# Kernel optimization log

Hardware: AMD Instinct MI355X
Metric: run time of the kernel (lower is better)

## Reference

```python
import jax, jax.numpy as jnp
import numpy as np

NUM_ITER = 5
ALPHA = 5.0   # spatial bandwidth, bilateral kernel
BETA = 5.0    # feature bandwidth, bilateral kernel
GAMMA = 5.0   # spatial bandwidth, spatial kernel
W_1 = 1.0
W_2 = 1.0


def setup_inputs() -> dict:
    key = jax.random.key(0)
    k1, k2 = jax.random.split(key)
    B, C, X, Y, Z = 1, 4, 32, 16, 16
    log_unary = jax.random.normal(k1, (B, C, X, Y, Z), dtype=jnp.float32)
    features_pairwise = jax.random.normal(k2, (B, 2, X, Y, Z), dtype=jnp.float32)
    # Potts-model compatibility: ones minus identity, [C_out, C_in] (conv1d kernel size 1)
    compatibility_weights = (jnp.ones((C, C)) - jnp.eye(C)).astype(jnp.float32)
    return {"log_unary": log_unary, "features_pairwise": features_pairwise,
            "compatibility_weights": compatibility_weights}


def _gauss_kernel(f):
    # f: [B, D, N] feature vectors; dense Gaussian filter matrix K_ij = exp(-||f_i-f_j||^2/2)
    sq = jnp.sum(f * f, axis=1)  # [B, N]
    d2 = sq[:, :, None] + sq[:, None, :] - 2.0 * jnp.einsum('bdn,bdm->bnm', f, f)
    return jnp.exp(-0.5 * jnp.maximum(d2, 0.0))  # [B, N, N]


def reference(log_unary, features_pairwise, compatibility_weights):
    B, C, X, Y, Z = log_unary.shape
    N = X * Y * Z
    lu = log_unary.reshape(B, C, N)
    q = jax.nn.softmax(lu, axis=1)

    gx, gy, gz = jnp.meshgrid(jnp.arange(X), jnp.arange(Y), jnp.arange(Z), indexing='ij')
    spatial = jnp.stack([gx, gy, gz], axis=0).astype(jnp.float32).reshape(1, 3, N)
    spatial = jnp.broadcast_to(spatial, (B, 3, N))
    img_fea = features_pairwise.reshape(B, features_pairwise.shape[1], N)

    f1 = jnp.concatenate([spatial / ALPHA, img_fea / BETA], axis=1)  # bilateral features
    f2 = spatial / GAMMA                                             # spatial features

    K1 = _gauss_kernel(f1)
    K2 = _gauss_kernel(f2)
    # norm = filter(ones) = row sums; scale = rsqrt(norm)
    scale1 = jax.lax.rsqrt(jnp.sum(K1, axis=2))[:, None, :]  # [B,1,N]
    scale2 = jax.lax.rsqrt(jnp.sum(K2, axis=2))[:, None, :]

    for _ in range(NUM_ITER):
        q1 = jnp.einsum('bnm,bcm->bcn', K1, q * scale1) * scale1
        q2 = jnp.einsum('bnm,bcm->bcn', K2, q * scale2) * scale2
        q_comb = W_1 * q1 + W_2 * q2
        q_update = jnp.einsum('oc,bcn->bon', compatibility_weights, q_comb)
        q = jax.nn.softmax(lu - q_update, axis=1)

    return q.reshape(B, C, X, Y, Z)
```

## Files before the change

kernel.cpp:

```cpp
#include <hip/hip_runtime.h>
#include <math.h>


constexpr int   NT    = 8192;
constexpr float SQL2E = 1.2011224087864498f;
constexpr float LOG2E = 1.4426950408889634f;
constexpr float INVA  = 0.2f * SQL2E;

constexpr int R_M = 0, R_U1 = 32, R_U2 = 36, R_S1 = 40, R_S2 = 41, R_CV = 42;

static __device__ __forceinline__ float ex2(float x) {
    return __builtin_amdgcn_exp2f(x);
}

__constant__ float INVSQF[7] = {1.f, 1.f, 0.70710678f, 0.40824829f,
                                0.20412415f, 0.09128709f, 0.03726780f};

__global__ __launch_bounds__(256) void k_setup(const float* __restrict__ feat,
                                               float* __restrict__ W) {
    int n = blockIdx.x * 256 + threadIdx.x;
    float g0 = feat[n] * 0.2f, g1 = feat[NT + n] * 0.2f;
    float eg = ex2(-0.5f * LOG2E * (g0*g0 + g1*g1));
    float p0[7], p1[7];
    p0[0] = 1.f; p1[0] = 1.f;
#pragma unroll
    for (int i = 1; i < 7; i++) { p0[i] = p0[i-1]*g0; p1[i] = p1[i-1]*g1; }
    int ab = 0;
#pragma unroll
    for (int k = 0; k <= 6; k++)
#pragma unroll
        for (int a = k; a >= 0; a--) {
            int b = k - a;
            W[(R_M + ab)*NT + n] = eg * p0[a]*INVSQF[a] * p1[b]*INVSQF[b];
            ab++;
        }
    int x = n >> 8, y = (n >> 4) & 15, z = n & 15;
    float Sx = 0.f, Sy = 0.f, Sz = 0.f;
    for (int j = 0; j < 32; j++) { float d = (float)(x-j)*INVA; Sx += ex2(-0.5f*d*d); }
    for (int j = 0; j < 16; j++) { float d = (float)(y-j)*INVA; Sy += ex2(-0.5f*d*d); }
    for (int j = 0; j < 16; j++) { float d = (float)(z-j)*INVA; Sz += ex2(-0.5f*d*d); }
    W[R_S2*NT + n] = rsqrtf(Sx * Sy * Sz);
}

__global__ __launch_bounds__(256) void k_conv(const float* __restrict__ W,
                                              float* __restrict__ Wout, int mode) {
    __shared__ float SP[512 * 17];
    const int idx = blockIdx.x;
    const int tid = threadIdx.x;
    if (mode == 0) {
        const float* src = W + (R_M + idx) * NT;
        for (int s = tid; s < NT; s += 256)
            SP[(s >> 4)*17 + (s & 15)] = src[s];
    } else if (idx < 112) {
        const float* Mr = W + (R_M + (idx >> 2)) * NT;
        const float* ur = W + (R_U1 + (idx & 3)) * NT;
        for (int s = tid; s < NT; s += 256)
            SP[(s >> 4)*17 + (s & 15)] = Mr[s] * ur[s];
    } else {
        const float* ur = W + (R_U2 + (idx - 112)) * NT;
        for (int s = tid; s < NT; s += 256)
            SP[(s >> 4)*17 + (s & 15)] = ur[s];
    }
    float g32[32];
#pragma unroll
    for (int d = 0; d < 32; d++) { float t = d * INVA; g32[d] = ex2(-0.5f*t*t); }
    __syncthreads();
#pragma unroll
    for (int rr = 0; rr < 2; rr++) {
        int r = tid + rr * 256;
        float v[16], acc[16];
#pragma unroll
        for (int z = 0; z < 16; z++) { v[z] = SP[r*17 + z]; acc[z] = 0.f; }
#pragma unroll
        for (int zp = 0; zp < 16; zp++)
#pragma unroll
            for (int z = 0; z < 16; z++) {
                int d = (z > zp) ? (z - zp) : (zp - z);
                acc[z] = fmaf(g32[d], v[zp], acc[z]);
            }
#pragma unroll
        for (int z = 0; z < 16; z++) SP[r*17 + z] = acc[z];
    }
    __syncthreads();
#pragma unroll
    for (int rr = 0; rr < 2; rr++) {
        int r = tid + rr * 256;
        int x = r >> 4, z = r & 15;
        int base = x * 272 + z;
        float v[16], acc[16];
#pragma unroll
        for (int y = 0; y < 16; y++) { v[y] = SP[base + y*17]; acc[y] = 0.f; }
#pragma unroll
        for (int yp = 0; yp < 16; yp++)
#pragma unroll
            for (int y = 0; y < 16; y++) {
                int d = (y > yp) ? (y - yp) : (yp - y);
                acc[y] = fmaf(g32[d], v[yp], acc[y]);
            }
#pragma unroll
        for (int y = 0; y < 16; y++) SP[base + y*17] = acc[y];
    }
    __syncthreads();
    {
        int base = (tid >> 4) * 17 + (tid & 15);
        float v[32], acc[32];
#pragma unroll
        for (int xp = 0; xp < 32; xp++) { v[xp] = SP[base + xp*272]; acc[xp] = 0.f; }
#pragma unroll
        for (int xp = 0; xp < 32; xp++)
#pragma unroll
            for (int x = 0; x < 32; x++) {
                int d = (x > xp) ? (x - xp) : (xp - x);
                acc[x] = fmaf(g32[d], v[xp], acc[x]);
            }
        float* outp = Wout + (R_CV + idx) * NT;
#pragma unroll
        for (int x = 0; x < 32; x++) outp[x*256 + tid] = acc[x];
    }
}

__global__ __launch_bounds__(256) void k_init(float* __restrict__ W,
                                              const float* __restrict__ lu) {
    int n = blockIdx.x * 256 + threadIdx.x;
    float rs = 0.f;
#pragma unroll
    for (int ab = 0; ab < 28; ab++)
        rs = fmaf(W[(R_M+ab)*NT + n], W[(R_CV+ab)*NT + n], rs);
    float s1 = rsqrtf(rs);
    float s2 = W[R_S2*NT + n];
    W[R_S1*NT + n] = s1;
    float l0 = lu[n], l1 = lu[NT+n], l2 = lu[2*NT+n], l3 = lu[3*NT+n];
    float mx = fmaxf(fmaxf(l0,l1), fmaxf(l2,l3));
    float q0 = __expf(l0-mx), q1 = __expf(l1-mx), q2 = __expf(l2-mx), q3 = __expf(l3-mx);
    float inv = 1.f / (q0+q1+q2+q3);
    q0*=inv; q1*=inv; q2*=inv; q3*=inv;
    W[(R_U1+0)*NT+n]=q0*s1; W[(R_U1+1)*NT+n]=q1*s1; W[(R_U1+2)*NT+n]=q2*s1; W[(R_U1+3)*NT+n]=q3*s1;
    W[(R_U2+0)*NT+n]=q0*s2; W[(R_U2+1)*NT+n]=q1*s2; W[(R_U2+2)*NT+n]=q2*s2; W[(R_U2+3)*NT+n]=q3*s2;
}

__global__ __launch_bounds__(256) void k_fuse(float* __restrict__ W,
        const float* __restrict__ lu, const float* __restrict__ compat,
        float* __restrict__ out) {
    int n = blockIdx.x * 256 + threadIdx.x;
    float s1 = W[R_S1*NT + n], s2 = W[R_S2*NT + n];
    float q1[4] = {0.f, 0.f, 0.f, 0.f};
#pragma unroll
    for (int ab = 0; ab < 28; ab++) {
        float m = W[(R_M+ab)*NT + n];
#pragma unroll
        for (int c = 0; c < 4; c++)
            q1[c] = fmaf(m, W[(R_CV + ab*4 + c)*NT + n], q1[c]);
    }
    float comb[4];
#pragma unroll
    for (int c = 0; c < 4; c++)
        comb[c] = s1 * q1[c] + s2 * W[(R_CV + 112 + c)*NT + n];
    float q[4];
#pragma unroll
    for (int o = 0; o < 4; o++) {
        float upd = 0.f;
#pragma unroll
        for (int c = 0; c < 4; c++) upd = fmaf(compat[o*4+c], comb[c], upd);
        q[o] = lu[o*NT+n] - upd;
    }
    float mx = fmaxf(fmaxf(q[0],q[1]), fmaxf(q[2],q[3]));
    float sum = 0.f;
#pragma unroll
    for (int c = 0; c < 4; c++) { q[c] = __expf(q[c]-mx); sum += q[c]; }
    float inv = 1.f / sum;
#pragma unroll
    for (int c = 0; c < 4; c++) {
        q[c] *= inv;
        out[c*NT+n]        = q[c];
        W[(R_U1+c)*NT+n]   = q[c]*s1;
        W[(R_U2+c)*NT+n]   = q[c]*s2;
    }
}

extern "C" void kernel_launch(void* const* d_in, const int* in_sizes, int n_in,
                              void* d_out, int out_size, void* d_ws, size_t ws_size,
                              hipStream_t stream) {
    const float* lu     = (const float*)d_in[0];
    const float* feat   = (const float*)d_in[1];
    const float* compat = (const float*)d_in[2];
    float* out = (float*)d_out;
    float* W   = (float*)d_ws;

    k_setup<<<dim3(32), dim3(256), 0, stream>>>(feat, W);
    k_conv <<<dim3(28), dim3(256), 0, stream>>>(W, W, 0);
    k_init <<<dim3(32), dim3(256), 0, stream>>>(W, lu);
    for (int it = 0; it < 5; it++) {
        k_conv<<<dim3(116), dim3(256), 0, stream>>>(W, W, 1);
        k_fuse<<<dim3(32),  dim3(256), 0, stream>>>(W, lu, compat, out);
    }
}
```

Baseline: 146.3 us.

## Fuse whole CRF pipeline into one cooperative kernel with grid syncs

Replaces the 13 separate kernel launches with a single cooperative persistent kernel of 116 blocks that uses grid.sync between the setup, init, conv and fuse phases. The setup moment computation is folded into the conv blocks, and fuse work is spread over all blocks at about 71 points each. It also skips the intermediate output writes except on the last iteration. The goal is to remove per-launch overhead and gaps between kernels, at the cost of grid-wide barrier latency and fewer active threads in the per-point phases; the old multi-kernel path remains as a fallback if the cooperative launch fails.

```diff
diff --git a/kernel.cpp b/kernel.cpp
--- a/kernel.cpp
+++ b/kernel.cpp
@@ -1,13 +1,18 @@
 #include <hip/hip_runtime.h>
+#include <hip/hip_cooperative_groups.h>
 #include <math.h>
 
+namespace cg = cooperative_groups;
+
 
 constexpr int   NT    = 8192;
+constexpr float LOG2E = 1.4426950408889634f;
 constexpr float SQL2E = 1.2011224087864498f;
-constexpr float LOG2E = 1.4426950408889634f;
 constexpr float INVA  = 0.2f * SQL2E;
 
 constexpr int R_M = 0, R_U1 = 32, R_U2 = 36, R_S1 = 40, R_S2 = 41, R_CV = 42;
+constexpr int NBLK = 116;
+constexpr int PPB  = (NT + NBLK - 1) / NBLK;
 
 static __device__ __forceinline__ float ex2(float x) {
     return __builtin_amdgcn_exp2f(x);
@@ -15,6 +20,190 @@
 
 __constant__ float INVSQF[7] = {1.f, 1.f, 0.70710678f, 0.40824829f,
                                 0.20412415f, 0.09128709f, 0.03726780f};
+__constant__ int AB_A[28] = {0, 1,0, 2,1,0, 3,2,1,0, 4,3,2,1,0,
+                             5,4,3,2,1,0, 6,5,4,3,2,1,0};
+__constant__ int AB_B[28] = {0, 0,1, 0,1,2, 0,1,2,3, 0,1,2,3,4,
+                             0,1,2,3,4,5, 0,1,2,3,4,5,6};
+
+static __device__ __forceinline__ void conv3d_store(float* SP,
+                                                    float* __restrict__ outp,
+                                                    int tid) {
+    float g32[32];
+#pragma unroll
+    for (int d = 0; d < 32; d++) { float t = d * INVA; g32[d] = ex2(-0.5f*t*t); }
+    __syncthreads();
+#pragma unroll
+    for (int rr = 0; rr < 2; rr++) {
+        int r = tid + rr * 256;
+        float v[16], acc[16];
+#pragma unroll
+        for (int z = 0; z < 16; z++) { v[z] = SP[r*17 + z]; acc[z] = 0.f; }
+#pragma unroll
+        for (int zp = 0; zp < 16; zp++)
+#pragma unroll
+            for (int z = 0; z < 16; z++) {
+                int d = (z > zp) ? (z - zp) : (zp - z);
+                acc[z] = fmaf(g32[d], v[zp], acc[z]);
+            }
+#pragma unroll
+        for (int z = 0; z < 16; z++) SP[r*17 + z] = acc[z];
+    }
+    __syncthreads();
+#pragma unroll
+    for (int rr = 0; rr < 2; rr++) {
+        int r = tid + rr * 256;
+        int x = r >> 4, z = r & 15;
+        int base = x * 272 + z;
+        float v[16], acc[16];
+#pragma unroll
+        for (int y = 0; y < 16; y++) { v[y] = SP[base + y*17]; acc[y] = 0.f; }
+#pragma unroll
+        for (int yp = 0; yp < 16; yp++)
+#pragma unroll
+            for (int y = 0; y < 16; y++) {
+                int d = (y > yp) ? (y - yp) : (yp - y);
+                acc[y] = fmaf(g32[d], v[yp], acc[y]);
+            }
+#pragma unroll
+        for (int y = 0; y < 16; y++) SP[base + y*17] = acc[y];
+    }
+    __syncthreads();
+    {
+        int base = (tid >> 4) * 17 + (tid & 15);
+        float v[32], acc[32];
+#pragma unroll
+        for (int xp = 0; xp < 32; xp++) { v[xp] = SP[base + xp*272]; acc[xp] = 0.f; }
+#pragma unroll
+        for (int xp = 0; xp < 32; xp++)
+#pragma unroll
+            for (int x = 0; x < 32; x++) {
+                int d = (x > xp) ? (x - xp) : (xp - x);
+                acc[x] = fmaf(g32[d], v[xp], acc[x]);
+            }
+#pragma unroll
+        for (int x = 0; x < 32; x++) outp[x*256 + tid] = acc[x];
+    }
+}
+
+static __device__ __forceinline__ void init_point(float* __restrict__ W,
+                                                  const float* __restrict__ lu,
+                                                  int n) {
+    float rs = 0.f;
+#pragma unroll
+    for (int ab = 0; ab < 28; ab++)
+        rs = fmaf(W[(R_M+ab)*NT + n], W[(R_CV+ab)*NT + n], rs);
+    float s1 = rsqrtf(rs);
+    float s2 = W[R_S2*NT + n];
+    W[R_S1*NT + n] = s1;
+    float l0 = lu[n], l1 = lu[NT+n], l2 = lu[2*NT+n], l3 = lu[3*NT+n];
+    float mx = fmaxf(fmaxf(l0,l1), fmaxf(l2,l3));
+    float q0 = __expf(l0-mx), q1 = __expf(l1-mx), q2 = __expf(l2-mx), q3 = __expf(l3-mx);
+    float inv = 1.f / (q0+q1+q2+q3);
+    q0*=inv; q1*=inv; q2*=inv; q3*=inv;
+    W[(R_U1+0)*NT+n]=q0*s1; W[(R_U1+1)*NT+n]=q1*s1; W[(R_U1+2)*NT+n]=q2*s1; W[(R_U1+3)*NT+n]=q3*s1;
+    W[(R_U2+0)*NT+n]=q0*s2; W[(R_U2+1)*NT+n]=q1*s2; W[(R_U2+2)*NT+n]=q2*s2; W[(R_U2+3)*NT+n]=q3*s2;
+}
+
+static __device__ __forceinline__ void fuse_point(float* __restrict__ W,
+        const float* __restrict__ lu, const float* __restrict__ compat,
+        float* __restrict__ out, int n, int last) {
+    float s1 = W[R_S1*NT + n], s2 = W[R_S2*NT + n];
+    float q1[4] = {0.f, 0.f, 0.f, 0.f};
+#pragma unroll
+    for (int ab = 0; ab < 28; ab++) {
+        float m = W[(R_M+ab)*NT + n];
+#pragma unroll
+        for (int c = 0; c < 4; c++)
+            q1[c] = fmaf(m, W[(R_CV + ab*4 + c)*NT + n], q1[c]);
+    }
+    float comb[4];
+#pragma unroll
+    for (int c = 0; c < 4; c++)
+        comb[c] = s1 * q1[c] + s2 * W[(R_CV + 112 + c)*NT + n];
+    float q[4];
+#pragma unroll
+    for (int o = 0; o < 4; o++) {
+        float upd = 0.f;
+#pragma unroll
+        for (int c = 0; c < 4; c++) upd = fmaf(compat[o*4+c], comb[c], upd);
+        q[o] = lu[o*NT+n] - upd;
+    }
+    float mx = fmaxf(fmaxf(q[0],q[1]), fmaxf(q[2],q[3]));
+    float sum = 0.f;
+#pragma unroll
+    for (int c = 0; c < 4; c++) { q[c] = __expf(q[c]-mx); sum += q[c]; }
+    float inv = 1.f / sum;
+    if (last) {
+#pragma unroll
+        for (int c = 0; c < 4; c++) out[c*NT+n] = q[c] * inv;
+    } else {
+#pragma unroll
+        for (int c = 0; c < 4; c++) {
+            float qq = q[c] * inv;
+            W[(R_U1+c)*NT+n] = qq*s1;
+            W[(R_U2+c)*NT+n] = qq*s2;
+        }
+    }
+}
+
+__global__ __launch_bounds__(256) void k_crf_all(const float* __restrict__ lu,
+        const float* __restrict__ feat, const float* __restrict__ compat,
+        float* __restrict__ out, float* __restrict__ W) {
+    cg::grid_group grid = cg::this_grid();
+    __shared__ float SP[512 * 17];
+    const int bid = blockIdx.x, tid = threadIdx.x;
+
+    if (bid < 28) {
+        const int a = AB_A[bid], b = AB_B[bid];
+        const float ca = INVSQF[a], cb = INVSQF[b];
+        for (int s = tid; s < NT; s += 256) {
+            float g0 = feat[s] * 0.2f, g1 = feat[NT + s] * 0.2f;
+            float eg = ex2(-0.5f * LOG2E * (g0*g0 + g1*g1));
+            float pa = 1.f;
+            for (int i = 0; i < a; i++) pa *= g0;
+            float pb = 1.f;
+            for (int i = 0; i < b; i++) pb *= g1;
+            float v = eg * pa * ca * pb * cb;
+            W[(R_M + bid)*NT + s] = v;
+            SP[(s >> 4)*17 + (s & 15)] = v;
+        }
+        conv3d_store(SP, W + (R_CV + bid)*NT, tid);
+    } else {
+        const int nb = (bid - 28) * 94 + tid;
+        if (tid < 94 && nb < NT) {
+            int x = nb >> 8, y = (nb >> 4) & 15, z = nb & 15;
+            float Sx = 0.f, Sy = 0.f, Sz = 0.f;
+            for (int j = 0; j < 32; j++) { float d = (float)(x-j)*INVA; Sx += ex2(-0.5f*d*d); }
+            for (int j = 0; j < 16; j++) { float d = (float)(y-j)*INVA; Sy += ex2(-0.5f*d*d); }
+            for (int j = 0; j < 16; j++) { float d = (float)(z-j)*INVA; Sz += ex2(-0.5f*d*d); }
+            W[R_S2*NT + nb] = rsqrtf(Sx * Sy * Sz);
+        }
+    }
+    grid.sync();
+
+    { int n = bid * PPB + tid; if (tid < PPB && n < NT) init_point(W, lu, n); }
+    grid.sync();
+
+    for (int it = 0; it < 5; ++it) {
+        {
+            const int idx = bid;
+            if (idx < 112) {
+                const float* Mr = W + (R_M + (idx >> 2))*NT;
+                const float* ur = W + (R_U1 + (idx & 3))*NT;
+                for (int s = tid; s < NT; s += 256)
+                    SP[(s >> 4)*17 + (s & 15)] = Mr[s] * ur[s];
+            } else {
+                const float* ur = W + (R_U2 + (idx - 112))*NT;
+                for (int s = tid; s < NT; s += 256)
+                    SP[(s >> 4)*17 + (s & 15)] = ur[s];
+            }
+            conv3d_store(SP, W + (R_CV + idx)*NT, tid);
+        }
+        grid.sync();
+        { int n = bid * PPB + tid; if (tid < PPB && n < NT) fuse_point(W, lu, compat, out, n, it == 4); }
+        grid.sync();
+    }
+}
 
 __global__ __launch_bounds__(256) void k_setup(const float* __restrict__ feat,
                                                float* __restrict__ W) {
@@ -61,120 +250,20 @@
         for (int s = tid; s < NT; s += 256)
             SP[(s >> 4)*17 + (s & 15)] = ur[s];
     }
-    float g32[32];
-#pragma unroll
-    for (int d = 0; d < 32; d++) { float t = d * INVA; g32[d] = ex2(-0.5f*t*t); }
-    __syncthreads();
-#pragma unroll
-    for (int rr = 0; rr < 2; rr++) {
-        int r = tid + rr * 256;
-        float v[16], acc[16];
-#pragma unroll
-        for (int z = 0; z < 16; z++) { v[z] = SP[r*17 + z]; acc[z] = 0.f; }
-#pragma unroll
-        for (int zp = 0; zp < 16; zp++)
-#pragma unroll
-            for (int z = 0; z < 16; z++) {
-                int d = (z > zp) ? (z - zp) : (zp - z);
-                acc[z] = fmaf(g32[d], v[zp], acc[z]);
-            }
-#pragma unroll
-        for (int z = 0; z < 16; z++) SP[r*17 + z] = acc[z];
-    }
-    __syncthreads();
-#pragma unroll
-    for (int rr = 0; rr < 2; rr++) {
-        int r = tid + rr * 256;
-        int x = r >> 4, z = r & 15;
-        int base = x * 272 + z;
-        float v[16], acc[16];
-#pragma unroll
-        for (int y = 0; y < 16; y++) { v[y] = SP[base + y*17]; acc[y] = 0.f; }
-#pragma unroll
-        for (int yp = 0; yp < 16; yp++)
-#pragma unroll
-            for (int y = 0; y < 16; y++) {
-                int d = (y > yp) ? (y - yp) : (yp - y);
-                acc[y] = fmaf(g32[d], v[yp], acc[y]);
-            }
-#pragma unroll
-        for (int y = 0; y < 16; y++) SP[base + y*17] = acc[y];
-    }
-    __syncthreads();
-    {
-        int base = (tid >> 4) * 17 + (tid & 15);
-        float v[32], acc[32];
-#pragma unroll
-        for (int xp = 0; xp < 32; xp++) { v[xp] = SP[base + xp*272]; acc[xp] = 0.f; }
-#pragma unroll
-        for (int xp = 0; xp < 32; xp++)
-#pragma unroll
-            for (int x = 0; x < 32; x++) {
-                int d = (x > xp) ? (x - xp) : (xp - x);
-                acc[x] = fmaf(g32[d], v[xp], acc[x]);
-            }
-        float* outp = Wout + (R_CV + idx) * NT;
-#pragma unroll
-        for (int x = 0; x < 32; x++) outp[x*256 + tid] = acc[x];
-    }
+    conv3d_store(SP, Wout + (R_CV + idx)*NT, tid);
 }
 
 __global__ __launch_bounds__(256) void k_init(float* __restrict__ W,
                                               const float* __restrict__ lu) {
     int n = blockIdx.x * 256 + threadIdx.x;
-    float rs = 0.f;
-#pragma unroll
-    for (int ab = 0; ab < 28; ab++)
-        rs = fmaf(W[(R_M+ab)*NT + n], W[(R_CV+ab)*NT + n], rs);
-    float s1 = rsqrtf(rs);
-    float s2 = W[R_S2*NT + n];
-    W[R_S1*NT + n] = s1;
-    float l0 = lu[n], l1 = lu[NT+n], l2 = lu[2*NT+n], l3 = lu[3*NT+n];
-    float mx = fmaxf(fmaxf(l0,l1), fmaxf(l2,l3));
-    float q0 = __expf(l0-mx), q1 = __expf(l1-mx), q2 = __expf(l2-mx), q3 = __expf(l3-mx);
-    float inv = 1.f / (q0+q1+q2+q3);
-    q0*=inv; q1*=inv; q2*=inv; q3*=inv;
-    W[(R_U1+0)*NT+n]=q0*s1; W[(R_U1+1)*NT+n]=q1*s1; W[(R_U1+2)*NT+n]=q2*s1; W[(R_U1+3)*NT+n]=q3*s1;
-    W[(R_U2+0)*NT+n]=q0*s2; W[(R_U2+1)*NT+n]=q1*s2; W[(R_U2+2)*NT+n]=q2*s2; W[(R_U2+3)*NT+n]=q3*s2;
+    init_point(W, lu, n);
 }
 
 __global__ __launch_bounds__(256) void k_fuse(float* __restrict__ W,
         const float* __restrict__ lu, const float* __restrict__ compat,
-        float* __restrict__ out) {
+        float* __restrict__ out, int last) {
     int n = blockIdx.x * 256 + threadIdx.x;
-    float s1 = W[R_S1*NT + n], s2 = W[R_S2*NT + n];
-    float q1[4] = {0.f, 0.f, 0.f, 0.f};
-#pragma unroll
-    for (int ab = 0; ab < 28; ab++) {
-        float m = W[(R_M+ab)*NT + n];
-#pragma unroll
-        for (int c = 0; c < 4; c++)
-            q1[c] = fmaf(m, W[(R_CV + ab*4 + c)*NT + n], q1[c]);
-    }
-    float comb[4];
-#pragma unroll
-    for (int c = 0; c < 4; c++)
-        comb[c] = s1 * q1[c] + s2 * W[(R_CV + 112 + c)*NT + n];
-    float q[4];
-#pragma unroll
-    for (int o = 0; o < 4; o++) {
-        float upd = 0.f;
-#pragma unroll
-        for (int c = 0; c < 4; c++) upd = fmaf(compat[o*4+c], comb[c], upd);
-        q[o] = lu[o*NT+n] - upd;
-    }
-    float mx = fmaxf(fmaxf(q[0],q[1]), fmaxf(q[2],q[3]));
-    float sum = 0.f;
-#pragma unroll
-    for (int c = 0; c < 4; c++) { q[c] = __expf(q[c]-mx); sum += q[c]; }
-    float inv = 1.f / sum;
-#pragma unroll
-    for (int c = 0; c < 4; c++) {
-        q[c] *= inv;
-        out[c*NT+n]        = q[c];
-        W[(R_U1+c)*NT+n]   = q[c]*s1;
-        W[(R_U2+c)*NT+n]   = q[c]*s2;
-    }
+    fuse_point(W, lu, compat, out, n, last);
 }
 
 extern "C" void kernel_launch(void* const* d_in, const int* in_sizes, int n_in,
@@ -186,11 +275,17 @@
     float* out = (float*)d_out;
     float* W   = (float*)d_ws;
 
-    k_setup<<<dim3(32), dim3(256), 0, stream>>>(feat, W);
-    k_conv <<<dim3(28), dim3(256), 0, stream>>>(W, W, 0);
-    k_init <<<dim3(32), dim3(256), 0, stream>>>(W, lu);
-    for (int it = 0; it < 5; it++) {
-        k_conv<<<dim3(116), dim3(256), 0, stream>>>(W, W, 1);
-        k_fuse<<<dim3(32),  dim3(256), 0, stream>>>(W, lu, compat, out);
-    }
-}
+    void* args[] = {(void*)&lu, (void*)&feat, (void*)&compat, (void*)&out, (void*)&W};
+    hipError_t rc = hipLaunchCooperativeKernel((const void*)k_crf_all,
+                                               dim3(NBLK), dim3(256), args, 0, stream);
+    if (rc != hipSuccess) {
+        (void)hipGetLastError();
+        k_setup<<<dim3(32), dim3(256), 0, stream>>>(feat, W);
+        k_conv <<<dim3(28), dim3(256), 0, stream>>>(W, W, 0);
+        k_init <<<dim3(32), dim3(256), 0, stream>>>(W, lu);
+        for (int it = 0; it < 5; it++) {
+            k_conv<<<dim3(116), dim3(256), 0, stream>>>(W, W, 1);
+            k_fuse<<<dim3(32),  dim3(256), 0, stream>>>(W, lu, compat, out, it == 4);
+        }
+    }
+}
```

Measured after the change: 443.7 us. 203% more time.

## Fuse setup into separable conv, use 512-thread conv blocks with vectorized loads

Applied to the files above, without the earlier changes.

Merges the setup and initial convolution kernels into one phase that computes each moment map and convolves it directly from shared memory. The spatial normalization moves into the init kernel. The separable 3D Gaussian convolution now runs with 512 threads per block, one row per thread, and the x pass is split into two halves. This raises parallelism and cuts per-thread register work. Conv input loads use float4, and the final fuse skips the workspace writes, giving one fewer launch and less memory traffic at the cost of more barrier-synchronized threads per block.

```diff
diff --git a/kernel.cpp b/kernel.cpp
--- a/kernel.cpp
+++ b/kernel.cpp
@@ -3,8 +3,8 @@
 
 
 constexpr int   NT    = 8192;
+constexpr float LOG2E = 1.4426950408889634f;
 constexpr float SQL2E = 1.2011224087864498f;
-constexpr float LOG2E = 1.4426950408889634f;
 constexpr float INVA  = 0.2f * SQL2E;
 
 constexpr int R_M = 0, R_U1 = 32, R_U2 = 36, R_S1 = 40, R_S2 = 41, R_CV = 42;
@@ -15,119 +15,120 @@
 
 __constant__ float INVSQF[7] = {1.f, 1.f, 0.70710678f, 0.40824829f,
                                 0.20412415f, 0.09128709f, 0.03726780f};
-
-__global__ __launch_bounds__(256) void k_setup(const float* __restrict__ feat,
-                                               float* __restrict__ W) {
+__constant__ int AB_A[28] = {0, 1,0, 2,1,0, 3,2,1,0, 4,3,2,1,0,
+                             5,4,3,2,1,0, 6,5,4,3,2,1,0};
+__constant__ int AB_B[28] = {0, 0,1, 0,1,2, 0,1,2,3, 0,1,2,3,4,
+                             0,1,2,3,4,5, 0,1,2,3,4,5,6};
+
+static __device__ __forceinline__ void conv3d_store512(float* SP,
+                                                       float* __restrict__ outp,
+                                                       int tid) {
+    float g32[32];
+#pragma unroll
+    for (int d = 0; d < 32; d++) { float t = d * INVA; g32[d] = ex2(-0.5f*t*t); }
+    __syncthreads();
+    {
+        int r = tid;
+        float v[16], acc[16];
+#pragma unroll
+        for (int z = 0; z < 16; z++) { v[z] = SP[r*17 + z]; acc[z] = 0.f; }
+#pragma unroll
+        for (int zp = 0; zp < 16; zp++)
+#pragma unroll
+            for (int z = 0; z < 16; z++) {
+                int d = (z > zp) ? (z - zp) : (zp - z);
+                acc[z] = fmaf(g32[d], v[zp], acc[z]);
+            }
+#pragma unroll
+        for (int z = 0; z < 16; z++) SP[r*17 + z] = acc[z];
+    }
+    __syncthreads();
+    {
+        int x = tid >> 4, z = tid & 15;
+        int base = x * 272 + z;
+        float v[16], acc[16];
+#pragma unroll
+        for (int y = 0; y < 16; y++) { v[y] = SP[base + y*17]; acc[y] = 0.f; }
+#pragma unroll
+        for (int yp = 0; yp < 16; yp++)
+#pragma unroll
+            for (int y = 0; y < 16; y++) {
+                int d = (y > yp) ? (y - yp) : (yp - y);
+                acc[y] = fmaf(g32[d], v[yp], acc[y]);
+            }
+#pragma unroll
+        for (int y = 0; y < 16; y++) SP[base + y*17] = acc[y];
+    }
+    __syncthreads();
+    {
+        int c = tid & 255, h = tid >> 8;
+        int base = (c >> 4) * 17 + (c & 15);
+        float v[32];
+#pragma unroll
+        for (int xp = 0; xp < 32; xp++) v[xp] = SP[base + xp*272];
+        float acc[16];
+#pragma unroll
+        for (int x0 = 0; x0 < 16; x0++) acc[x0] = 0.f;
+        if (h == 0) {
+#pragma unroll
+            for (int xp = 0; xp < 32; xp++)
+#pragma unroll
+                for (int x0 = 0; x0 < 16; x0++) {
+                    int d = (x0 > xp) ? (x0 - xp) : (xp - x0);
+                    acc[x0] = fmaf(g32[d], v[xp], acc[x0]);
+                }
+#pragma unroll
+            for (int x0 = 0; x0 < 16; x0++) outp[x0*256 + c] = acc[x0];
+        } else {
+#pragma unroll
+            for (int xp = 0; xp < 32; xp++)
+#pragma unroll
+                for (int x0 = 0; x0 < 16; x0++) {
+                    int x = x0 + 16;
+                    int d = (x > xp) ? (x - xp) : (xp - x);
+                    acc[x0] = fmaf(g32[d], v[xp], acc[x0]);
+                }
+#pragma unroll
+            for (int x0 = 0; x0 < 16; x0++) outp[(x0+16)*256 + c] = acc[x0];
+        }
+    }
+}
+
+__global__ __launch_bounds__(512) void k_phaseA(const float* __restrict__ feat,
+                                                float* __restrict__ W) {
+    __shared__ float SP[512 * 17];
+    const int bid = blockIdx.x, tid = threadIdx.x;
+    const int a = AB_A[bid], b = AB_B[bid];
+    const float ca = INVSQF[a], cb = INVSQF[b];
+    for (int s = tid; s < NT; s += 512) {
+        float g0 = feat[s] * 0.2f, g1 = feat[NT + s] * 0.2f;
+        float eg = ex2(-0.5f * LOG2E * (g0*g0 + g1*g1));
+        float pa = 1.f;
+        for (int i = 0; i < a; i++) pa *= g0;
+        float pb = 1.f;
+        for (int i = 0; i < b; i++) pb *= g1;
+        float v = eg * pa * ca * pb * cb;
+        W[(R_M + bid)*NT + s] = v;
+        SP[(s >> 4)*17 + (s & 15)] = v;
+    }
+    conv3d_store512(SP, W + (R_CV + bid)*NT, tid);
+}
+
+__global__ __launch_bounds__(256) void k_init(float* __restrict__ W,
+                                              const float* __restrict__ lu) {
     int n = blockIdx.x * 256 + threadIdx.x;
-    float g0 = feat[n] * 0.2f, g1 = feat[NT + n] * 0.2f;
-    float eg = ex2(-0.5f * LOG2E * (g0*g0 + g1*g1));
-    float p0[7], p1[7];
-    p0[0] = 1.f; p1[0] = 1.f;
-#pragma unroll
-    for (int i = 1; i < 7; i++) { p0[i] = p0[i-1]*g0; p1[i] = p1[i-1]*g1; }
-    int ab = 0;
-#pragma unroll
-    for (int k = 0; k <= 6; k++)
-#pragma unroll
-        for (int a = k; a >= 0; a--) {
-            int b = k - a;
-            W[(R_M + ab)*NT + n] = eg * p0[a]*INVSQF[a] * p1[b]*INVSQF[b];
-            ab++;
-        }
     int x = n >> 8, y = (n >> 4) & 15, z = n & 15;
     float Sx = 0.f, Sy = 0.f, Sz = 0.f;
     for (int j = 0; j < 32; j++) { float d = (float)(x-j)*INVA; Sx += ex2(-0.5f*d*d); }
     for (int j = 0; j < 16; j++) { float d = (float)(y-j)*INVA; Sy += ex2(-0.5f*d*d); }
     for (int j = 0; j < 16; j++) { float d = (float)(z-j)*INVA; Sz += ex2(-0.5f*d*d); }
-    W[R_S2*NT + n] = rsqrtf(Sx * Sy * Sz);
-}
-
-__global__ __launch_bounds__(256) void k_conv(const float* __restrict__ W,
-                                              float* __restrict__ Wout, int mode) {
-    __shared__ float SP[512 * 17];
-    const int idx = blockIdx.x;
-    const int tid = threadIdx.x;
-    if (mode == 0) {
-        const float* src = W + (R_M + idx) * NT;
-        for (int s = tid; s < NT; s += 256)
-            SP[(s >> 4)*17 + (s & 15)] = src[s];
-    } else if (idx < 112) {
-        const float* Mr = W + (R_M + (idx >> 2)) * NT;
-        const float* ur = W + (R_U1 + (idx & 3)) * NT;
-        for (int s = tid; s < NT; s += 256)
-            SP[(s >> 4)*17 + (s & 15)] = Mr[s] * ur[s];
-    } else {
-        const float* ur = W + (R_U2 + (idx - 112)) * NT;
-        for (int s = tid; s < NT; s += 256)
-            SP[(s >> 4)*17 + (s & 15)] = ur[s];
-    }
-    float g32[32];
-#pragma unroll
-    for (int d = 0; d < 32; d++) { float t = d * INVA; g32[d] = ex2(-0.5f*t*t); }
-    __syncthreads();
-#pragma unroll
-    for (int rr = 0; rr < 2; rr++) {
-        int r = tid + rr * 256;
-        float v[16], acc[16];
-#pragma unroll
-        for (int z = 0; z < 16; z++) { v[z] = SP[r*17 + z]; acc[z] = 0.f; }
-#pragma unroll
-        for (int zp = 0; zp < 16; zp++)
-#pragma unroll
-            for (int z = 0; z < 16; z++) {
-                int d = (z > zp) ? (z - zp) : (zp - z);
-                acc[z] = fmaf(g32[d], v[zp], acc[z]);
-            }
-#pragma unroll
-        for (int z = 0; z < 16; z++) SP[r*17 + z] = acc[z];
-    }
-    __syncthreads();
-#pragma unroll
-    for (int rr = 0; rr < 2; rr++) {
-        int r = tid + rr * 256;
-        int x = r >> 4, z = r & 15;
-        int base = x * 272 + z;
-        float v[16], acc[16];
-#pragma unroll
-        for (int y = 0; y < 16; y++) { v[y] = SP[base + y*17]; acc[y] = 0.f; }
-#pragma unroll
-        for (int yp = 0; yp < 16; yp++)
-#pragma unroll
-            for (int y = 0; y < 16; y++) {
-                int d = (y > yp) ? (y - yp) : (yp - y);
-                acc[y] = fmaf(g32[d], v[yp], acc[y]);
-            }
-#pragma unroll
-        for (int y = 0; y < 16; y++) SP[base + y*17] = acc[y];
-    }
-    __syncthreads();
-    {
-        int base = (tid >> 4) * 17 + (tid & 15);
-        float v[32], acc[32];
-#pragma unroll
-        for (int xp = 0; xp < 32; xp++) { v[xp] = SP[base + xp*272]; acc[xp] = 0.f; }
-#pragma unroll
-        for (int xp = 0; xp < 32; xp++)
-#pragma unroll
-            for (int x = 0; x < 32; x++) {
-                int d = (x > xp) ? (x - xp) : (xp - x);
-                acc[x] = fmaf(g32[d], v[xp], acc[x]);
-            }
-        float* outp = Wout + (R_CV + idx) * NT;
-#pragma unroll
-        for (int x = 0; x < 32; x++) outp[x*256 + tid] = acc[x];
-    }
-}
-
-__global__ __launch_bounds__(256) void k_init(float* __restrict__ W,
-                                              const float* __restrict__ lu) {
-    int n = blockIdx.x * 256 + threadIdx.x;
+    float s2 = rsqrtf(Sx * Sy * Sz);
+    W[R_S2*NT + n] = s2;
     float rs = 0.f;
 #pragma unroll
     for (int ab = 0; ab < 28; ab++)
         rs = fmaf(W[(R_M+ab)*NT + n], W[(R_CV+ab)*NT + n], rs);
     float s1 = rsqrtf(rs);
-    float s2 = W[R_S2*NT + n];
     W[R_S1*NT + n] = s1;
     float l0 = lu[n], l1 = lu[NT+n], l2 = lu[2*NT+n], l3 = lu[3*NT+n];
     float mx = fmaxf(fmaxf(l0,l1), fmaxf(l2,l3));
@@ -138,9 +139,40 @@
     W[(R_U2+0)*NT+n]=q0*s2; W[(R_U2+1)*NT+n]=q1*s2; W[(R_U2+2)*NT+n]=q2*s2; W[(R_U2+3)*NT+n]=q3*s2;
 }
 
+__global__ __launch_bounds__(512) void k_conv(const float* __restrict__ W,
+                                              float* __restrict__ Wout) {
+    __shared__ float SP[512 * 17];
+    const int idx = blockIdx.x;
+    const int tid = threadIdx.x;
+    if (idx < 112) {
+        const float4* M4 = (const float4*)(W + (R_M + (idx >> 2))*NT);
+        const float4* U4 = (const float4*)(W + (R_U1 + (idx & 3))*NT);
+#pragma unroll
+        for (int i = 0; i < 4; i++) {
+            int s4 = tid + i*512;
+            float4 m = M4[s4], u = U4[s4];
+            int s = s4 << 2;
+            int base = (s >> 4)*17 + (s & 15);
+            SP[base+0] = m.x*u.x; SP[base+1] = m.y*u.y;
+            SP[base+2] = m.z*u.z; SP[base+3] = m.w*u.w;
+        }
+    } else {
+        const float4* U4 = (const float4*)(W + (R_U2 + (idx - 112))*NT);
+#pragma unroll
+        for (int i = 0; i < 4; i++) {
+            int s4 = tid + i*512;
+            float4 u = U4[s4];
+            int s = s4 << 2;
+            int base = (s >> 4)*17 + (s & 15);
+            SP[base+0] = u.x; SP[base+1] = u.y; SP[base+2] = u.z; SP[base+3] = u.w;
+        }
+    }
+    conv3d_store512(SP, Wout + (R_CV + idx)*NT, tid);
+}
+
 __global__ __launch_bounds__(256) void k_fuse(float* __restrict__ W,
         const float* __restrict__ lu, const float* __restrict__ compat,
-        float* __restrict__ out) {
+        float* __restrict__ out, int last) {
     int n = blockIdx.x * 256 + threadIdx.x;
     float s1 = W[R_S1*NT + n], s2 = W[R_S2*NT + n];
     float q1[4] = {0.f, 0.f, 0.f, 0.f};
@@ -168,12 +200,16 @@
 #pragma unroll
     for (int c = 0; c < 4; c++) { q[c] = __expf(q[c]-mx); sum += q[c]; }
     float inv = 1.f / sum;
-#pragma unroll
-    for (int c = 0; c < 4; c++) {
-        q[c] *= inv;
-        out[c*NT+n]        = q[c];
-        W[(R_U1+c)*NT+n]   = q[c]*s1;
-        W[(R_U2+c)*NT+n]   = q[c]*s2;
+    if (last) {
+#pragma unroll
+        for (int c = 0; c < 4; c++) out[c*NT+n] = q[c] * inv;
+    } else {
+#pragma unroll
+        for (int c = 0; c < 4; c++) {
+            float qq = q[c] * inv;
+            W[(R_U1+c)*NT+n] = qq*s1;
+            W[(R_U2+c)*NT+n] = qq*s2;
+        }
     }
 }
 
@@ -186,11 +222,10 @@
     float* out = (float*)d_out;
     float* W   = (float*)d_ws;
 
-    k_setup<<<dim3(32), dim3(256), 0, stream>>>(feat, W);
-    k_conv <<<dim3(28), dim3(256), 0, stream>>>(W, W, 0);
-    k_init <<<dim3(32), dim3(256), 0, stream>>>(W, lu);
+    k_phaseA<<<dim3(28),  dim3(512), 0, stream>>>(feat, W);
+    k_init  <<<dim3(32),  dim3(256), 0, stream>>>(W, lu);
     for (int it = 0; it < 5; it++) {
-        k_conv<<<dim3(116), dim3(256), 0, stream>>>(W, W, 1);
-        k_fuse<<<dim3(32),  dim3(256), 0, stream>>>(W, lu, compat, out);
-    }
-}
+        k_conv<<<dim3(116), dim3(512), 0, stream>>>(W, W);
+        k_fuse<<<dim3(32),  dim3(256), 0, stream>>>(W, lu, compat, out, it == 4);
+    }
+}
```

After: 139.6 us. 4.6% less time.
